# Kernel tuning notes

Measured on AMD Instinct MI355X. Metric: run time of the kernel, lower is better.

## Reference

```python
import jax, jax.numpy as jnp
import numpy as np

S = 2048   # sample_batch
N = 16     # num_h (agents per sample group)
OBS = 8
PRED = 12
H = 16     # hidden / embed size


def _lstm_cell(x, h, c, Wi, Wh, b):
    # torch LSTMCell gate order: i, f, g, o
    g = x @ Wi + h @ Wh + b
    i, f, gg, o = jnp.split(g, 4, axis=-1)
    c = jax.nn.sigmoid(f) * c + jax.nn.sigmoid(i) * jnp.tanh(gg)
    h = jax.nn.sigmoid(o) * jnp.tanh(c)
    return h, c


def setup_inputs() -> dict:
    key = jax.random.key(0)
    ks = jax.random.split(key, 16)
    B = S * N
    p = lambda k, sh: jax.random.normal(k, sh, jnp.float32) * 0.1
    return dict(
        traj_rel=jax.random.normal(ks[0], (OBS, B, 2), jnp.float32),
        obs_traj_pos=jax.random.normal(ks[1], (OBS, B, 2), jnp.float32),
        nei_index=jax.random.randint(ks[2], (B, N), 0, 2, jnp.int32),
        noise=jax.random.normal(ks[3], (PRED, B, 2), jnp.float32),
        enc_emb_W=p(ks[4], (2, H)), enc_emb_b=jnp.zeros((H,), jnp.float32),
        enc_Wi=p(ks[5], (H, 4 * H)), enc_Wh=p(ks[6], (H, 4 * H)), enc_b=jnp.zeros((4 * H,), jnp.float32),
        dec_in_W=p(ks[7], (H + 2, H)), dec_in_b=jnp.zeros((H,), jnp.float32),
        dec_Wi=p(ks[8], (H, 4 * H)), dec_Wh=p(ks[9], (H, 4 * H)), dec_b=jnp.zeros((4 * H,), jnp.float32),
        pool_rel_W=p(ks[10], (2, H)), pool_rel_b=jnp.zeros((H,), jnp.float32),
        pool_mlp_W=p(ks[11], (2 * H, H)), pool_mlp_b=jnp.zeros((H,), jnp.float32),
        out_W=p(ks[12], (H, 4)), out_b=jnp.zeros((4,), jnp.float32),
    )


def reference(traj_rel, obs_traj_pos, nei_index, noise,
              enc_emb_W, enc_emb_b, enc_Wi, enc_Wh, enc_b,
              dec_in_W, dec_in_b, dec_Wi, dec_Wh, dec_b,
              pool_rel_W, pool_rel_b, pool_mlp_W, pool_mlp_b,
              out_W, out_b):
    B = traj_rel.shape[1]
    mask = nei_index > 0  # (B, N)

    # --- history encoder: embed + LSTM over obs steps, take last hidden ---
    def enc_step(carry, x):
        h, c = carry
        e = jax.nn.relu(x @ enc_emb_W + enc_emb_b)
        h, c = _lstm_cell(e, h, c, enc_Wi, enc_Wh, enc_b)
        return (h, c), None

    h0 = jnp.zeros((B, H), traj_rel.dtype)
    (h_enc, _), _ = jax.lax.scan(enc_step, (h0, h0), traj_rel[:OBS])

    # --- neighbor pooling: embed relative pos, concat neighbor hidden, MLP, masked max-pool ---
    def pool(rel, h):
        re = jax.nn.relu(rel @ pool_rel_W + pool_rel_b)  # (B, N, H)
        hn = jnp.broadcast_to(h.reshape(S, 1, N, H), (S, N, N, H)).reshape(B, N, H)
        feat = jax.nn.relu(jnp.concatenate([re, hn], -1) @ pool_mlp_W + pool_mlp_b)
        masked = jnp.where(mask[..., None], feat, -1e9)
        pooled = masked.max(axis=1)  # (B, H)
        has = mask.any(axis=1, keepdims=True)
        return jnp.where(has, pooled, 0.0)

    def dec_step(carry, noise_t):
        h, c, ctx, out, pos = carry
        inp = jax.lax.stop_gradient(jnp.concatenate([ctx, out], -1))  # .detach() in torch
        e = jax.nn.relu(inp @ dec_in_W + dec_in_b)
        h, c = _lstm_cell(e, h, c, dec_Wi, dec_Wh, dec_b)
        p = pos.reshape(S, N, 2)
        # rel[s,i,j] = pos[s,i] - pos[s,j]  (matches expand/transpose subtraction)
        rel = (p[:, :, None, :] - p[:, None, :, :]).reshape(B, N, 2)
        ctx = pool(rel, h)
        o4 = (h + ctx) @ out_W + out_b
        mu = o4[:, :2]
        scale = jnp.clip(o4[:, 2:], -9.0, 4.0)
        std = jnp.exp(scale)
        pred = mu + std * noise_t
        pos = jax.lax.stop_gradient(pos + pred)
        return (h, c, ctx, pred, pos), (pred, mu, std)

    init = (h_enc, jnp.zeros_like(h_enc), jnp.zeros_like(h_enc),
            traj_rel[OBS - 1], obs_traj_pos[-1])
    _, (pred, mu, std) = jax.lax.scan(dec_step, init, noise)
    return pred, mu, std  # each (PRED, B, 2)
```

## Files before the change

### kernel.cpp

```cpp
#include <hip/hip_runtime.h>

#define S_    2048
#define N_    16
#define OBS_  8
#define PRED_ 12
#define B_    (S_*N_)
#define SCN_  2

typedef __attribute__((ext_vector_type(8))) short short8;
typedef __attribute__((ext_vector_type(4))) float floatx4;
typedef __attribute__((ext_vector_type(4))) unsigned uintx4;
typedef unsigned short ushort_t;

__device__ __forceinline__ float sigmf(float x) { return __builtin_amdgcn_rcpf(1.0f + __expf(-x)); }
__device__ __forceinline__ float tanhx(float x) { return fmaf(-2.0f, __builtin_amdgcn_rcpf(1.0f + __expf(2.0f*x)), 1.0f); }
__device__ __forceinline__ unsigned bfhi(float f) {
  return __builtin_bit_cast(unsigned, f) + 0x8000u;
}
__device__ __forceinline__ unsigned pack2bf(float lo, float hi) {
  return __builtin_amdgcn_perm(bfhi(hi), bfhi(lo), 0x07060302);
}
__device__ __forceinline__ ushort_t f2bf1(float f) { return (ushort_t)(bfhi(f) >> 16); }

extern "C" __global__ __launch_bounds__(128, 2) void traj_ar_kernel(
    const float* __restrict__ traj_rel, const float* __restrict__ obs_pos,
    const int*  __restrict__ nei,       const float* __restrict__ noise,
    const float* __restrict__ eeW, const float* __restrict__ eeb,
    const float* __restrict__ eWi, const float* __restrict__ eWh, const float* __restrict__ eb,
    const float* __restrict__ diW, const float* __restrict__ dib,
    const float* __restrict__ dWi, const float* __restrict__ dWh, const float* __restrict__ db,
    const float* __restrict__ prW, const float* __restrict__ prb,
    const float* __restrict__ mW,  const float* __restrict__ mb,
    const float* __restrict__ oW,  const float* __restrict__ ob,
    float* __restrict__ out)
{
  __shared__ __align__(16) float h_s[SCN_][256];
  __shared__ __align__(16) float ctx_s[SCN_][256];
  __shared__ __align__(16) ushort_t e_w[SCN_][384];
  __shared__ __align__(16) ushort_t h_w[SCN_][384];
  __shared__ __align__(16) ushort_t ctx_bf[SCN_][384];
  __shared__ __align__(16) float posx_s[SCN_][16];
  __shared__ __align__(16) float posy_s[SCN_][16];
  __shared__ __align__(16) ushort_t prev_bf[SCN_][32];
  __shared__            unsigned sm_s[SCN_][16];

  const int tid = threadIdx.x;
  const int w  = tid >> 6;
  const int l  = tid & 63;
  const int lq = l >> 4;
  const int lc = l & 15;
  const int u0 = lq*4;
  const int s  = blockIdx.x*SCN_ + w;

  {
    unsigned* hz = (unsigned*)h_w[w];
    unsigned* cz = (unsigned*)ctx_bf[w];
    hz[l] = 0; hz[64+l] = 0; hz[128+l] = 0;
    cz[l] = 0; cz[64+l] = 0; cz[128+l] = 0;
  }
  if (l < 32) {
    const int a = l >> 1, c = l & 1;
    float pv = traj_rel[((OBS_-1)*B_ + s*N_ + a)*2 + c];
    prev_bf[w][a*2+c] = f2bf1(pv);
    float po = obs_pos[((OBS_-1)*B_ + s*N_ + a)*2 + c];
    if (c == 0) posx_s[w][a] = po; else posy_s[w][a] = po;
  }
  {
    const int a = l >> 2, nb = (l & 3)*4;
    const int4 nv = *(const int4*)&nei[(s*N_ + a)*N_ + nb];
    unsigned bits = 0;
    bits |= (nv.x > 0) ? (1u << (nb+0)) : 0u;
    bits |= (nv.y > 0) ? (1u << (nb+1)) : 0u;
    bits |= (nv.z > 0) ? (1u << (nb+2)) : 0u;
    bits |= (nv.w > 0) ? (1u << (nb+3)) : 0u;
    bits |= __shfl_xor(bits, 1, 64);
    bits |= __shfl_xor(bits, 2, 64);
    if ((l & 3) == 0) sm_s[w][a] = bits;
  }

  short8 bfrag;
  {
    uintx4 bw;
    #pragma unroll
    for (int p = 0; p < 4; ++p)
      bw[p] = pack2bf(mW[(8*lq + 2*p)*16 + lc], mW[(8*lq + 2*p + 1)*16 + lc]);
    bfrag = __builtin_bit_cast(short8, bw);
  }
  const float bm = mb[lc];

  float pWx[8], pWy[8], pB[8];
  {
    const int wu0 = (lq & 1) * 8;
    #pragma unroll
    for (int j = 0; j < 8; ++j) {
      pWx[j] = prW[wu0 + j];
      pWy[j] = prW[16 + wu0 + j];
      pB[j]  = prb[wu0 + j];
    }
  }

  float oWc[16];
  #pragma unroll
  for (int m = 0; m < 16; ++m) oWc[m] = oW[m*4 + lq];
  const float obia = ob[lq];

  float ew0[4], ew1[4], ebv[4];
  #pragma unroll
  for (int r = 0; r < 4; ++r) {
    ew0[r] = eeW[u0+r]; ew1[r] = eeW[16+u0+r]; ebv[r] = eeb[u0+r];
  }

  const int row0 = (lq & 1) * 8;

  #define LOAD_GATE_FRAG(A, C, Wi_, Wh_, bias_, g) {                                      \
    const float* gsrc_ = (lq & 2) ? (Wh_) : (Wi_);                                        \
    uintx4 aw_;                                                                           \
    aw_[0] = pack2bf(gsrc_[(row0+0)*64 + (g)*16 + lc], gsrc_[(row0+1)*64 + (g)*16 + lc]); \
    aw_[1] = pack2bf(gsrc_[(row0+2)*64 + (g)*16 + lc], gsrc_[(row0+3)*64 + (g)*16 + lc]); \
    aw_[2] = pack2bf(gsrc_[(row0+4)*64 + (g)*16 + lc], gsrc_[(row0+5)*64 + (g)*16 + lc]); \
    aw_[3] = pack2bf(gsrc_[(row0+6)*64 + (g)*16 + lc], gsrc_[(row0+7)*64 + (g)*16 + lc]); \
    (A) = __builtin_bit_cast(short8, aw_);                                                \
    (C)[0] = (bias_)[(g)*16 + u0 + 0]; (C)[1] = (bias_)[(g)*16 + u0 + 1];                 \
    (C)[2] = (bias_)[(g)*16 + u0 + 2]; (C)[3] = (bias_)[(g)*16 + u0 + 3];                 \
  }

  short8 eA0, eA1, eA2, eA3; floatx4 eC0, eC1, eC2, eC3;
  LOAD_GATE_FRAG(eA0, eC0, eWi, eWh, eb, 0);
  LOAD_GATE_FRAG(eA1, eC1, eWi, eWh, eb, 1);
  LOAD_GATE_FRAG(eA2, eC2, eWi, eWh, eb, 2);
  LOAD_GATE_FRAG(eA3, eC3, eWi, eWh, eb, 3);

  #define LSTM_EW(r, hv) {                                                            \
    float ig = sigmf(dI[r]), fg = sigmf(dF[r]), gv = tanhx(dG[r]), og = sigmf(dO[r]); \
    c4[r] = fg*c4[r] + ig*gv;                                                         \
    hv = og * tanhx(c4[r]);                                                           \
  }

  floatx4 c4 = {0.0f, 0.0f, 0.0f, 0.0f};
  const float2* xr2 = (const float2*)traj_rel;
  for (int t = 0; t < OBS_; ++t) {
    float2 x = xr2[t*B_ + s*N_ + lc];
    float e0 = fmaxf(fmaf(x.y, ew1[0], fmaf(x.x, ew0[0], ebv[0])), 0.0f);
    float e1 = fmaxf(fmaf(x.y, ew1[1], fmaf(x.x, ew0[1], ebv[1])), 0.0f);
    float e2 = fmaxf(fmaf(x.y, ew1[2], fmaf(x.x, ew0[2], ebv[2])), 0.0f);
    float e3 = fmaxf(fmaf(x.y, ew1[3], fmaf(x.x, ew0[3], ebv[3])), 0.0f);
    uint2 ep; ep.x = pack2bf(e0, e1); ep.y = pack2bf(e2, e3);
    *(uint2*)&e_w[w][lc*24 + u0] = ep;
    const ushort_t* bp = (lq < 2) ? &e_w[w][lc*24 + (lq&1)*8] : &h_w[w][lc*24 + (lq&1)*8];
    short8 bfr = *(const short8*)bp;
    floatx4 dI = __builtin_amdgcn_mfma_f32_16x16x32_bf16(eA0, bfr, eC0, 0, 0, 0);
    floatx4 dF = __builtin_amdgcn_mfma_f32_16x16x32_bf16(eA1, bfr, eC1, 0, 0, 0);
    floatx4 dG = __builtin_amdgcn_mfma_f32_16x16x32_bf16(eA2, bfr, eC2, 0, 0, 0);
    floatx4 dO = __builtin_amdgcn_mfma_f32_16x16x32_bf16(eA3, bfr, eC3, 0, 0, 0);
    float h40, h41, h42, h43;
    LSTM_EW(0, h40); LSTM_EW(1, h41); LSTM_EW(2, h42); LSTM_EW(3, h43);
    uint2 hp2; hp2.x = pack2bf(h40, h41); hp2.y = pack2bf(h42, h43);
    *(uint2*)&h_w[w][lc*24 + u0] = hp2;
  }

  short8 dA0, dA1, dA2, dA3; floatx4 dC0, dC1, dC2, dC3;
  LOAD_GATE_FRAG(dA0, dC0, dWi, dWh, db, 0);
  LOAD_GATE_FRAG(dA1, dC1, dWi, dWh, db, 1);
  LOAD_GATE_FRAG(dA2, dC2, dWi, dWh, db, 2);
  LOAD_GATE_FRAG(dA3, dC3, dWi, dWh, db, 3);

  short8 diA; floatx4 diC;
  {
    uintx4 aw; aw[0]=0; aw[1]=0; aw[2]=0; aw[3]=0;
    if (lq < 2) {
      const int r0 = lq*8;
      #pragma unroll
      for (int p = 0; p < 4; ++p)
        aw[p] = pack2bf(diW[(r0+2*p)*16 + lc], diW[(r0+2*p+1)*16 + lc]);
    } else if (lq == 2) {
      aw[0] = pack2bf(diW[16*16 + lc], diW[17*16 + lc]);
    }
    diA = __builtin_bit_cast(short8, aw);
    #pragma unroll
    for (int r = 0; r < 4; ++r) diC[r] = dib[u0 + r];
  }

  floatx4 cm[16];
  #pragma unroll
  for (int tt = 0; tt < 16; ++tt) {
    const unsigned mi = sm_s[w][tt];
    #pragma unroll
    for (int r = 0; r < 4; ++r)
      cm[tt][r] = ((mi >> (u0 + r)) & 1u) ? bm : -1e9f;
  }

  c4 = (floatx4){0.0f, 0.0f, 0.0f, 0.0f};
  const int MU_OFF = PRED_*B_*2;
  const int SD_OFF = 2*PRED_*B_*2;
  for (int t = 0; t < PRED_; ++t) {
    const float nz = noise[(t*B_ + s*N_ + lc)*2 + (lq&1)];
    const floatx4 PX0 = *(const floatx4*)&posx_s[w][0];
    const floatx4 PX1 = *(const floatx4*)&posx_s[w][4];
    const floatx4 PX2 = *(const floatx4*)&posx_s[w][8];
    const floatx4 PX3 = *(const floatx4*)&posx_s[w][12];
    const floatx4 PY0 = *(const floatx4*)&posy_s[w][0];
    const floatx4 PY1 = *(const floatx4*)&posy_s[w][4];
    const floatx4 PY2 = *(const floatx4*)&posy_s[w][8];
    const floatx4 PY3 = *(const floatx4*)&posy_s[w][12];
    const float mx = posx_s[w][lc];
    const float my = posy_s[w][lc];
    {
      short8 cv = *(const short8*)&ctx_bf[w][lc*24 + (lq&1)*8];
      uintx4 pz; pz[0] = *(const unsigned*)&prev_bf[w][lc*2]; pz[1]=0; pz[2]=0; pz[3]=0;
      short8 pv = __builtin_bit_cast(short8, pz);
      short8 zz = {0,0,0,0,0,0,0,0};
      short8 bf1 = (lq < 2) ? cv : ((lq == 2) ? pv : zz);
      floatx4 d = __builtin_amdgcn_mfma_f32_16x16x32_bf16(diA, bf1, diC, 0, 0, 0);
      uint2 ep;
      ep.x = pack2bf(fmaxf(d[0],0.0f), fmaxf(d[1],0.0f));
      ep.y = pack2bf(fmaxf(d[2],0.0f), fmaxf(d[3],0.0f));
      *(uint2*)&e_w[w][lc*24 + u0] = ep;
    }
    {
      const ushort_t* bp = (lq < 2) ? &e_w[w][lc*24 + (lq&1)*8] : &h_w[w][lc*24 + (lq&1)*8];
      short8 bfr = *(const short8*)bp;
      floatx4 dI = __builtin_amdgcn_mfma_f32_16x16x32_bf16(dA0, bfr, dC0, 0, 0, 0);
      floatx4 dF = __builtin_amdgcn_mfma_f32_16x16x32_bf16(dA1, bfr, dC1, 0, 0, 0);
      floatx4 dG = __builtin_amdgcn_mfma_f32_16x16x32_bf16(dA2, bfr, dC2, 0, 0, 0);
      floatx4 dO = __builtin_amdgcn_mfma_f32_16x16x32_bf16(dA3, bfr, dC3, 0, 0, 0);
      float h40, h41, h42, h43;
      LSTM_EW(0, h40); LSTM_EW(1, h41); LSTM_EW(2, h42); LSTM_EW(3, h43);
      uint2 hp2; hp2.x = pack2bf(h40, h41); hp2.y = pack2bf(h42, h43);
      *(uint2*)&h_w[w][lc*24 + u0] = hp2;
      floatx4 hv4; hv4[0]=h40; hv4[1]=h41; hv4[2]=h42; hv4[3]=h43;
      *(floatx4*)&h_s[w][lc*16 + u0] = hv4;
    }
    const short8 hfrag = *(const short8*)&h_w[w][lc*24 + (lq&1)*8];
    {
      #pragma unroll
      for (int tt = 0; tt < 16; ++tt) {
        const floatx4 PXq = (tt<4)?PX0:(tt<8)?PX1:(tt<12)?PX2:PX3;
        const floatx4 PYq = (tt<4)?PY0:(tt<8)?PY1:(tt<12)?PY2:PY3;
        const float rx = PXq[tt&3] - mx;
        const float ry = PYq[tt&3] - my;
        float rr[8];
        #pragma unroll
        for (int j = 0; j < 8; ++j)
          rr[j] = fmaxf(fmaf(ry, pWy[j], fmaf(rx, pWx[j], pB[j])), 0.0f);
        uintx4 aw;
        aw[0] = pack2bf(rr[0], rr[1]);
        aw[1] = pack2bf(rr[2], rr[3]);
        aw[2] = pack2bf(rr[4], rr[5]);
        aw[3] = pack2bf(rr[6], rr[7]);
        const short8 refrag = __builtin_bit_cast(short8, aw);
        short8 a = (lq < 2) ? refrag : hfrag;
        floatx4 d = __builtin_amdgcn_mfma_f32_16x16x32_bf16(a, bfrag, cm[tt], 0, 0, 0);
        float pm = fmaxf(fmaxf(d[0], d[1]), fmaxf(d[2], d[3]));
        pm = fmaxf(pm, __shfl_xor(pm, 16, 64));
        pm = fmaxf(pm, __shfl_xor(pm, 32, 64));
        if (lq == (tt & 3)) {
          float cvv = fmaxf(pm, 0.0f);
          ctx_s[w][tt*16 + lc] = cvv;
          ctx_bf[w][tt*24 + lc] = f2bf1(cvv);
        }
      }
    }
    {
      float acc = obia;
      const floatx4* hp4 = (const floatx4*)&h_s[w][lc*16];
      const floatx4* cx4 = (const floatx4*)&ctx_s[w][lc*16];
      #pragma unroll
      for (int mm = 0; mm < 4; ++mm) {
        floatx4 hv = hp4[mm];
        floatx4 cv = cx4[mm];
        #pragma unroll
        for (int r = 0; r < 4; ++r)
          acc = fmaf(hv[r]+cv[r], oWc[mm*4+r], acc);
      }
      float sc = __shfl_down(acc, 32, 64);
      if (lq < 2) {
        float mu = acc;
        float scale = fminf(fmaxf(sc, -9.0f), 4.0f);
        float sd = __expf(scale);
        float pr = fmaf(sd, nz, mu);
        int o = (t*B_ + s*N_ + lc)*2 + lq;
        out[o]          = pr;
        out[MU_OFF + o] = mu;
        out[SD_OFF + o] = sd;
        if (lq == 0) posx_s[w][lc] = mx + pr;
        else         posy_s[w][lc] = my + pr;
        prev_bf[w][lc*2+lq] = f2bf1(pr);
      }
    }
  }
  #undef LSTM_EW
  #undef LOAD_GATE_FRAG
}

extern "C" void kernel_launch(void* const* d_in, const int* in_sizes, int n_in,
                              void* d_out, int out_size, void* d_ws, size_t ws_size,
                              hipStream_t stream) {
  (void)in_sizes; (void)n_in; (void)d_ws; (void)ws_size; (void)out_size;
  traj_ar_kernel<<<dim3(S_/SCN_), dim3(128), 0, stream>>>(
      (const float*)d_in[0],  (const float*)d_in[1],  (const int*)d_in[2],   (const float*)d_in[3],
      (const float*)d_in[4],  (const float*)d_in[5],  (const float*)d_in[6], (const float*)d_in[7],
      (const float*)d_in[8],  (const float*)d_in[9],  (const float*)d_in[10],(const float*)d_in[11],
      (const float*)d_in[12], (const float*)d_in[13], (const float*)d_in[14],(const float*)d_in[15],
      (const float*)d_in[16], (const float*)d_in[17], (const float*)d_in[18],(const float*)d_in[19],
      (float*)d_out);
}
```

Before: 166.9 us.

## Keep agent positions in registers and split pool relative-embedding work across half-waves

```diff
diff --git a/kernel.cpp b/kernel.cpp
--- a/kernel.cpp
+++ b/kernel.cpp
@@ -21,6 +21,9 @@
   return __builtin_amdgcn_perm(bfhi(hi), bfhi(lo), 0x07060302);
 }
 __device__ __forceinline__ ushort_t f2bf1(float f) { return (ushort_t)(bfhi(f) >> 16); }
+__device__ __forceinline__ float rlanef(float v, int lane) {
+  return __builtin_bit_cast(float, __builtin_amdgcn_readlane(__builtin_bit_cast(int, v), lane));
+}
 
 extern "C" __global__ __launch_bounds__(128, 2) void traj_ar_kernel(
     const float* __restrict__ traj_rel, const float* __restrict__ obs_pos,
@@ -39,9 +42,6 @@
   __shared__ __align__(16) ushort_t e_w[SCN_][384];
   __shared__ __align__(16) ushort_t h_w[SCN_][384];
   __shared__ __align__(16) ushort_t ctx_bf[SCN_][384];
-  __shared__ __align__(16) float posx_s[SCN_][16];
-  __shared__ __align__(16) float posy_s[SCN_][16];
-  __shared__ __align__(16) ushort_t prev_bf[SCN_][32];
   __shared__            unsigned sm_s[SCN_][16];
 
   const int tid = threadIdx.x;
@@ -51,6 +51,7 @@
   const int lc = l & 15;
   const int u0 = lq*4;
   const int s  = blockIdx.x*SCN_ + w;
+  const bool hi_half = (lq >= 2);
 
   {
     unsigned* hz = (unsigned*)h_w[w];
@@ -58,12 +59,13 @@
     hz[l] = 0; hz[64+l] = 0; hz[128+l] = 0;
     cz[l] = 0; cz[64+l] = 0; cz[128+l] = 0;
   }
-  if (l < 32) {
-    const int a = l >> 1, c = l & 1;
-    float pv = traj_rel[((OBS_-1)*B_ + s*N_ + a)*2 + c];
-    prev_bf[w][a*2+c] = f2bf1(pv);
-    float po = obs_pos[((OBS_-1)*B_ + s*N_ + a)*2 + c];
-    if (c == 0) posx_s[w][a] = po; else posy_s[w][a] = po;
+  float POSX = obs_pos[((OBS_-1)*B_ + s*N_ + lc)*2 + 0];
+  float POSY = obs_pos[((OBS_-1)*B_ + s*N_ + lc)*2 + 1];
+  unsigned prevu;
+  {
+    float pvx = traj_rel[((OBS_-1)*B_ + s*N_ + lc)*2 + 0];
+    float pvy = traj_rel[((OBS_-1)*B_ + s*N_ + lc)*2 + 1];
+    prevu = pack2bf(pvx, pvy);
   }
   {
     const int a = l >> 2, nb = (l & 3)*4;
@@ -194,19 +196,15 @@
   const int SD_OFF = 2*PRED_*B_*2;
   for (int t = 0; t < PRED_; ++t) {
     const float nz = noise[(t*B_ + s*N_ + lc)*2 + (lq&1)];
-    const floatx4 PX0 = *(const floatx4*)&posx_s[w][0];
-    const floatx4 PX1 = *(const floatx4*)&posx_s[w][4];
-    const floatx4 PX2 = *(const floatx4*)&posx_s[w][8];
-    const floatx4 PX3 = *(const floatx4*)&posx_s[w][12];
-    const floatx4 PY0 = *(const floatx4*)&posy_s[w][0];
-    const floatx4 PY1 = *(const floatx4*)&posy_s[w][4];
-    const floatx4 PY2 = *(const floatx4*)&posy_s[w][8];
-    const floatx4 PY3 = *(const floatx4*)&posy_s[w][12];
-    const float mx = posx_s[w][lc];
-    const float my = posy_s[w][lc];
+    float PXs[16], PYs[16];
+    #pragma unroll
+    for (int a2 = 0; a2 < 16; ++a2) {
+      PXs[a2] = rlanef(POSX, a2);
+      PYs[a2] = rlanef(POSY, a2);
+    }
     {
       short8 cv = *(const short8*)&ctx_bf[w][lc*24 + (lq&1)*8];
-      uintx4 pz; pz[0] = *(const unsigned*)&prev_bf[w][lc*2]; pz[1]=0; pz[2]=0; pz[3]=0;
+      uintx4 pz; pz[0] = prevu; pz[1]=0; pz[2]=0; pz[3]=0;
       short8 pv = __builtin_bit_cast(short8, pz);
       short8 zz = {0,0,0,0,0,0,0,0};
       short8 bf1 = (lq < 2) ? cv : ((lq == 2) ? pv : zz);
@@ -233,30 +231,51 @@
     const short8 hfrag = *(const short8*)&h_w[w][lc*24 + (lq&1)*8];
     {
       #pragma unroll
-      for (int tt = 0; tt < 16; ++tt) {
-        const floatx4 PXq = (tt<4)?PX0:(tt<8)?PX1:(tt<12)?PX2:PX3;
-        const floatx4 PYq = (tt<4)?PY0:(tt<8)?PY1:(tt<12)?PY2:PY3;
-        const float rx = PXq[tt&3] - mx;
-        const float ry = PYq[tt&3] - my;
+      for (int p = 0; p < 8; ++p) {
+        const int t0 = 2*p, t1 = 2*p + 1;
+        float rx0 = PXs[t0] - POSX, ry0 = PYs[t0] - POSY;
+        float rx1 = PXs[t1] - POSX, ry1 = PYs[t1] - POSY;
+        float rx = hi_half ? rx1 : rx0;
+        float ry = hi_half ? ry1 : ry0;
         float rr[8];
         #pragma unroll
         for (int j = 0; j < 8; ++j)
           rr[j] = fmaxf(fmaf(ry, pWy[j], fmaf(rx, pWx[j], pB[j])), 0.0f);
-        uintx4 aw;
-        aw[0] = pack2bf(rr[0], rr[1]);
-        aw[1] = pack2bf(rr[2], rr[3]);
-        aw[2] = pack2bf(rr[4], rr[5]);
-        aw[3] = pack2bf(rr[6], rr[7]);
-        const short8 refrag = __builtin_bit_cast(short8, aw);
-        short8 a = (lq < 2) ? refrag : hfrag;
-        floatx4 d = __builtin_amdgcn_mfma_f32_16x16x32_bf16(a, bfrag, cm[tt], 0, 0, 0);
-        float pm = fmaxf(fmaxf(d[0], d[1]), fmaxf(d[2], d[3]));
-        pm = fmaxf(pm, __shfl_xor(pm, 16, 64));
-        pm = fmaxf(pm, __shfl_xor(pm, 32, 64));
-        if (lq == (tt & 3)) {
-          float cvv = fmaxf(pm, 0.0f);
-          ctx_s[w][tt*16 + lc] = cvv;
-          ctx_bf[w][tt*24 + lc] = f2bf1(cvv);
+        unsigned a0 = pack2bf(rr[0], rr[1]);
+        unsigned a1 = pack2bf(rr[2], rr[3]);
+        unsigned a2 = pack2bf(rr[4], rr[5]);
+        unsigned a3 = pack2bf(rr[6], rr[7]);
+        unsigned s0 = __shfl_xor(a0, 32, 64);
+        unsigned s1 = __shfl_xor(a1, 32, 64);
+        unsigned s2 = __shfl_xor(a2, 32, 64);
+        unsigned s3 = __shfl_xor(a3, 32, 64);
+        uintx4 f0; f0[0]=a0; f0[1]=a1; f0[2]=a2; f0[3]=a3;
+        uintx4 f1; f1[0]=s0; f1[1]=s1; f1[2]=s2; f1[3]=s3;
+        const short8 reA = __builtin_bit_cast(short8, f0);
+        const short8 reB = __builtin_bit_cast(short8, f1);
+        {
+          short8 a = hi_half ? hfrag : reA;
+          floatx4 d = __builtin_amdgcn_mfma_f32_16x16x32_bf16(a, bfrag, cm[t0], 0, 0, 0);
+          float pm = fmaxf(fmaxf(d[0], d[1]), fmaxf(d[2], d[3]));
+          pm = fmaxf(pm, __shfl_xor(pm, 16, 64));
+          pm = fmaxf(pm, __shfl_xor(pm, 32, 64));
+          if (lq == (t0 & 3)) {
+            float cvv = fmaxf(pm, 0.0f);
+            ctx_s[w][t0*16 + lc] = cvv;
+            ctx_bf[w][t0*24 + lc] = f2bf1(cvv);
+          }
+        }
+        {
+          short8 a = hi_half ? hfrag : reB;
+          floatx4 d = __builtin_amdgcn_mfma_f32_16x16x32_bf16(a, bfrag, cm[t1], 0, 0, 0);
+          float pm = fmaxf(fmaxf(d[0], d[1]), fmaxf(d[2], d[3]));
+          pm = fmaxf(pm, __shfl_xor(pm, 16, 64));
+          pm = fmaxf(pm, __shfl_xor(pm, 32, 64));
+          if (lq == (t1 & 3)) {
+            float cvv = fmaxf(pm, 0.0f);
+            ctx_s[w][t1*16 + lc] = cvv;
+            ctx_bf[w][t1*24 + lc] = f2bf1(cvv);
+          }
         }
       }
     }
@@ -273,19 +292,21 @@
           acc = fmaf(hv[r]+cv[r], oWc[mm*4+r], acc);
       }
       float sc = __shfl_down(acc, 32, 64);
+      float mu = acc;
+      float scale = fminf(fmaxf(sc, -9.0f), 4.0f);
+      float sd = __expf(scale);
+      float pr = fmaf(sd, nz, mu);
       if (lq < 2) {
-        float mu = acc;
-        float scale = fminf(fmaxf(sc, -9.0f), 4.0f);
-        float sd = __expf(scale);
-        float pr = fmaf(sd, nz, mu);
         int o = (t*B_ + s*N_ + lc)*2 + lq;
         out[o]          = pr;
         out[MU_OFF + o] = mu;
         out[SD_OFF + o] = sd;
-        if (lq == 0) posx_s[w][lc] = mx + pr;
-        else         posy_s[w][lc] = my + pr;
-        prev_bf[w][lc*2+lq] = f2bf1(pr);
       }
+      float prx = __shfl(pr, lc, 64);
+      float pry = __shfl(pr, 16 + lc, 64);
+      POSX += prx;
+      POSY += pry;
+      prevu = pack2bf(prx, pry);
     }
   }
   #undef LSTM_EW
```

Result: faster. 160.0 us (-4.1%).
